# Kernel optimization log

Measured on AMD Instinct MI355X. Metric: run time of the kernel, lower is better.

Reference implementation:

```python
import jax, jax.numpy as jnp
import numpy as np

NUM_EMBEDDINGS = 512
EMBEDDING_DIM = 64


def setup_inputs() -> dict:
    key = jax.random.key(0)
    k1, k2 = jax.random.split(key)
    x = jax.random.normal(k1, (32, EMBEDDING_DIM, 64, 64), dtype=jnp.float32)
    # codebook init: uniform(-1/K, 1/K) as in the torch module
    lim = 1.0 / NUM_EMBEDDINGS
    embedding = jax.random.uniform(k2, (NUM_EMBEDDINGS, EMBEDDING_DIM), dtype=jnp.float32,
                                   minval=-lim, maxval=lim)
    return {"x": x, "embedding": embedding}


def reference(x, embedding):
    # x: [B, D, H, W]; embedding: [K, D]
    B, D, H, W = x.shape
    xp = jnp.transpose(x, (0, 2, 3, 1))            # [B, H, W, D]
    flat = xp.reshape(-1, D)                        # [N, D]
    dists = (jnp.sum(flat * flat, axis=-1, keepdims=True)
             - 2.0 * (flat @ embedding.T)
             + jnp.sum(embedding * embedding, axis=-1))
    latents = jnp.argmin(dists, axis=-1)            # [N]
    q = embedding[latents].reshape(B, H, W, D)      # gather codebook
    q = jnp.transpose(q, (0, 3, 1, 2))              # [B, D, H, W]
    # quantized_st and quantized are numerically identical in forward;
    # they differ only in gradient routing (straight-through vs codebook).
    return (q, q)
```

## Files before the change

### kernel.cpp

```cpp
#include <hip/hip_runtime.h>

#define NUM_EMB 512
#define DIM 64
#define HW 4096
#define NPOS 131072
#define XELEMS 8388608

__global__ void vq_esq_kernel(const float* __restrict__ e, float* __restrict__ esq) {
    int k = blockIdx.x * blockDim.x + threadIdx.x;
    if (k < NUM_EMB) {
        const float4* er = reinterpret_cast<const float4*>(e + k * DIM);
        float s = 0.f;
#pragma unroll
        for (int i = 0; i < DIM / 4; ++i) {
            float4 v = er[i];
            s += v.x * v.x + v.y * v.y + v.z * v.z + v.w * v.w;
        }
        esq[k] = s;
    }
}

__global__ __launch_bounds__(256)
__attribute__((amdgpu_waves_per_eu(2, 2)))
void vq_main_kernel(const float* __restrict__ x,
                    const float* __restrict__ e,
                    const float* __restrict__ esq,
                    float* __restrict__ out) {
    int n = blockIdx.x * 256 + threadIdx.x;
    int b = n >> 12;
    int hw = n & 4095;

    const float* xb = x + (size_t)b * (DIM * HW) + hw;

    float xr[DIM];
#pragma unroll
    for (int d = 0; d < DIM; ++d) {
        xr[d] = xb[(size_t)d * HW];
    }
#pragma unroll
    for (int d = 0; d < DIM; d += 8) {
        asm volatile("" : "+v"(xr[d + 0]), "+v"(xr[d + 1]), "+v"(xr[d + 2]),
                          "+v"(xr[d + 3]), "+v"(xr[d + 4]), "+v"(xr[d + 5]),
                          "+v"(xr[d + 6]), "+v"(xr[d + 7]));
    }

    float xsq = 0.f;
#pragma unroll
    for (int d = 0; d < DIM; ++d) xsq = fmaf(xr[d], xr[d], xsq);

    float best = 3.4e38f;
    int bestk = 0;

    for (int k = 0; k < NUM_EMB; ++k) {
        const float* ek = e + k * DIM;
        float d0 = 0.f, d1 = 0.f, d2 = 0.f, d3 = 0.f;
#pragma unroll
        for (int d = 0; d < DIM; d += 4) {
            d0 = fmaf(xr[d + 0], ek[d + 0], d0);
            d1 = fmaf(xr[d + 1], ek[d + 1], d1);
            d2 = fmaf(xr[d + 2], ek[d + 2], d2);
            d3 = fmaf(xr[d + 3], ek[d + 3], d3);
        }
        float dot = (d0 + d1) + (d2 + d3);
        float dist = fmaf(-2.f, dot, xsq) + esq[k];
        if (dist < best) {
            best = dist;
            bestk = k;
        }
    }

    const float4* eb = reinterpret_cast<const float4*>(e + bestk * DIM);
    float* o0 = out + (size_t)b * (DIM * HW) + hw;
    float* o1 = o0 + XELEMS;
#pragma unroll
    for (int i = 0; i < DIM / 4; ++i) {
        float4 v = eb[i];
        o0[(size_t)(4 * i + 0) * HW] = v.x;
        o0[(size_t)(4 * i + 1) * HW] = v.y;
        o0[(size_t)(4 * i + 2) * HW] = v.z;
        o0[(size_t)(4 * i + 3) * HW] = v.w;
        o1[(size_t)(4 * i + 0) * HW] = v.x;
        o1[(size_t)(4 * i + 1) * HW] = v.y;
        o1[(size_t)(4 * i + 2) * HW] = v.z;
        o1[(size_t)(4 * i + 3) * HW] = v.w;
    }
}

extern "C" void kernel_launch(void* const* d_in, const int* in_sizes, int n_in,
                              void* d_out, int out_size, void* d_ws, size_t ws_size,
                              hipStream_t stream) {
    const float* x = (const float*)d_in[0];
    const float* e = (const float*)d_in[1];
    float* out = (float*)d_out;
    float* esq = (float*)d_ws;

    vq_esq_kernel<<<1, NUM_EMB, 0, stream>>>(e, esq);
    vq_main_kernel<<<NPOS / 256, 256, 0, stream>>>(x, e, esq, out);
}
```

Measured before the change: 301.3 us.

## Split codebook search across two half-blocks with double-buffered row loads

Each block now handles 128 positions with 256 threads. Each half of the threads scans half of the codebook, and the two partial argmins are merged through shared memory. Codebook rows are loaded as float4 into two alternating register buffers, so the next row's load overlaps the current row's FMAs. Each half then writes one of the two output copies. This doubles the thread count to raise parallelism and hide latency, at the cost of loading x twice and higher register pressure from the buffers. Tie-breaking stays consistent because the lower half wins on equal distances.

```diff
diff --git a/kernel.cpp b/kernel.cpp
--- a/kernel.cpp
+++ b/kernel.cpp
@@ -5,6 +5,8 @@
 #define HW 4096
 #define NPOS 131072
 #define XELEMS 8388608
+#define KHALF 256
+#define POSB 128
 
 __global__ void vq_esq_kernel(const float* __restrict__ e, float* __restrict__ esq) {
     int k = blockIdx.x * blockDim.x + threadIdx.x;
@@ -26,17 +28,22 @@
                     const float* __restrict__ e,
                     const float* __restrict__ esq,
                     float* __restrict__ out) {
-    int n = blockIdx.x * 256 + threadIdx.x;
-    int b = n >> 12;
-    int hw = n & 4095;
+    __shared__ float s_best[2][POSB];
+    __shared__ int s_bk[2][POSB];
 
-    const float* xb = x + (size_t)b * (DIM * HW) + hw;
+    const int t = threadIdx.x;
+    const int half = t >> 7;
+    const int tl = t & 127;
+
+    const int pbase = blockIdx.x * POSB;
+    const int b = pbase >> 12;
+    const int hwb = pbase & 4095;
+
+    const float* xb = x + (size_t)b * (DIM * HW) + (hwb + tl);
 
     float xr[DIM];
 #pragma unroll
-    for (int d = 0; d < DIM; ++d) {
-        xr[d] = xb[(size_t)d * HW];
-    }
+    for (int d = 0; d < DIM; ++d) xr[d] = xb[(size_t)d * HW];
 #pragma unroll
     for (int d = 0; d < DIM; d += 8) {
         asm volatile("" : "+v"(xr[d + 0]), "+v"(xr[d + 1]), "+v"(xr[d + 2]),
@@ -49,40 +56,62 @@
     for (int d = 0; d < DIM; ++d) xsq = fmaf(xr[d], xr[d], xsq);
 
     float best = 3.4e38f;
-    int bestk = 0;
+    int bk = 0;
+    const int kbeg = half * KHALF;
+    const int klast = kbeg + KHALF - 1;
 
-    for (int k = 0; k < NUM_EMB; ++k) {
-        const float* ek = e + k * DIM;
-        float d0 = 0.f, d1 = 0.f, d2 = 0.f, d3 = 0.f;
+    auto loadrow = [&](float4* buf, int krow) {
+        int off = krow * (DIM * 4);
+        asm volatile("" : "+v"(off));
+        const float4* ek4 =
+            reinterpret_cast<const float4*>(reinterpret_cast<const char*>(e) + off);
 #pragma unroll
-        for (int d = 0; d < DIM; d += 4) {
-            d0 = fmaf(xr[d + 0], ek[d + 0], d0);
-            d1 = fmaf(xr[d + 1], ek[d + 1], d1);
-            d2 = fmaf(xr[d + 2], ek[d + 2], d2);
-            d3 = fmaf(xr[d + 3], ek[d + 3], d3);
+        for (int j = 0; j < 16; ++j) buf[j] = ek4[j];
+    };
+    auto fmarow = [&](const float4* buf, int krow) {
+        float a0 = 0.f, a1 = 0.f, a2 = 0.f, a3 = 0.f;
+#pragma unroll
+        for (int j = 0; j < 16; ++j) {
+            a0 = fmaf(xr[4 * j + 0], buf[j].x, a0);
+            a1 = fmaf(xr[4 * j + 1], buf[j].y, a1);
+            a2 = fmaf(xr[4 * j + 2], buf[j].z, a2);
+            a3 = fmaf(xr[4 * j + 3], buf[j].w, a3);
         }
-        float dot = (d0 + d1) + (d2 + d3);
-        float dist = fmaf(-2.f, dot, xsq) + esq[k];
-        if (dist < best) {
-            best = dist;
-            bestk = k;
-        }
+        float dot = (a0 + a1) + (a2 + a3);
+        float dist = fmaf(-2.f, dot, xsq) + esq[krow];
+        if (dist < best) { best = dist; bk = krow; }
+    };
+
+    float4 bufA[16], bufB[16];
+    loadrow(bufA, kbeg);
+    for (int kk = 0; kk < KHALF; kk += 2) {
+        int k0 = kbeg + kk;
+        loadrow(bufB, k0 + 1);
+        fmarow(bufA, k0);
+        int kn = (k0 + 2 > klast) ? klast : k0 + 2;
+        loadrow(bufA, kn);
+        fmarow(bufB, k0 + 1);
     }
 
-    const float4* eb = reinterpret_cast<const float4*>(e + bestk * DIM);
-    float* o0 = out + (size_t)b * (DIM * HW) + hw;
-    float* o1 = o0 + XELEMS;
+    s_best[half][tl] = best;
+    s_bk[half][tl] = bk;
+    __syncthreads();
+
+    float bl = s_best[0][tl];
+    int kl = s_bk[0][tl];
+    float bu = s_best[1][tl];
+    int ku = s_bk[1][tl];
+    int kw = (bu < bl) ? ku : kl;
+
+    const float4* eb = reinterpret_cast<const float4*>(e + kw * DIM);
+    float* o = out + (size_t)half * XELEMS + (size_t)b * (DIM * HW) + (hwb + tl);
 #pragma unroll
     for (int i = 0; i < DIM / 4; ++i) {
         float4 v = eb[i];
-        o0[(size_t)(4 * i + 0) * HW] = v.x;
-        o0[(size_t)(4 * i + 1) * HW] = v.y;
-        o0[(size_t)(4 * i + 2) * HW] = v.z;
-        o0[(size_t)(4 * i + 3) * HW] = v.w;
-        o1[(size_t)(4 * i + 0) * HW] = v.x;
-        o1[(size_t)(4 * i + 1) * HW] = v.y;
-        o1[(size_t)(4 * i + 2) * HW] = v.z;
-        o1[(size_t)(4 * i + 3) * HW] = v.w;
+        o[(size_t)(4 * i + 0) * HW] = v.x;
+        o[(size_t)(4 * i + 1) * HW] = v.y;
+        o[(size_t)(4 * i + 2) * HW] = v.z;
+        o[(size_t)(4 * i + 3) * HW] = v.w;
     }
 }
 
@@ -95,5 +124,5 @@
     float* esq = (float*)d_ws;
 
     vq_esq_kernel<<<1, NUM_EMB, 0, stream>>>(e, esq);
-    vq_main_kernel<<<NPOS / 256, 256, 0, stream>>>(x, e, esq, out);
+    vq_main_kernel<<<NPOS / POSB, 256, 0, stream>>>(x, e, esq, out);
 }
```

After: 599.5 us. 98.9% more time.
